# Performance work log

Hardware: AMD Instinct MI355X
Metric: run time of the kernel (lower is better)

The kernel has to match this reference:

```python
import jax, jax.numpy as jnp
import numpy as np

DIM = 3072
NUM_HEADS = 24
HEAD_DIM = 128
SEQ = 2048
BATCH = 1
EPS = 1e-6


def _make_rope(seq_len: int, head_dim: int):
    # Standard RoPE angles; cos/sin laid out per interleaved-pair convention
    # (each frequency repeated for the (real, imag) pair), shape [S, head_dim].
    half = head_dim // 2
    inv_freq = 1.0 / (10000.0 ** (np.arange(0, half, dtype=np.float32) / half))
    t = np.arange(seq_len, dtype=np.float32)
    freqs = np.outer(t, inv_freq)  # [S, half]
    freqs = np.repeat(freqs, 2, axis=-1)  # [S, head_dim], pairs share the angle
    return jnp.asarray(np.cos(freqs)), jnp.asarray(np.sin(freqs))


def setup_inputs() -> dict:
    key = jax.random.key(0)
    ks = jax.random.split(key, 8)
    inner = NUM_HEADS * HEAD_DIM
    s = 0.02
    hidden_states = jax.random.normal(ks[0], (BATCH, SEQ, DIM), dtype=jnp.float32)
    wq = jax.random.normal(ks[1], (inner, DIM), dtype=jnp.float32) * s
    wk = jax.random.normal(ks[2], (inner, DIM), dtype=jnp.float32) * s
    wv = jax.random.normal(ks[3], (inner, DIM), dtype=jnp.float32) * s
    bq = jax.random.normal(ks[4], (inner,), dtype=jnp.float32) * s
    bk = jax.random.normal(ks[5], (inner,), dtype=jnp.float32) * s
    bv = jax.random.normal(ks[6], (inner,), dtype=jnp.float32) * s
    norm_q_w = jnp.ones((HEAD_DIM,), dtype=jnp.float32)
    norm_k_w = jnp.ones((HEAD_DIM,), dtype=jnp.float32)
    cos, sin = _make_rope(SEQ, HEAD_DIM)
    return {
        "hidden_states": hidden_states,
        "wq": wq, "bq": bq, "wk": wk, "bk": bk, "wv": wv, "bv": bv,
        "norm_q_w": norm_q_w, "norm_k_w": norm_k_w,
        "cos": cos, "sin": sin,
    }


def _rms_norm(x, w, eps=EPS):
    # RMSNorm over the last (head_dim) axis.
    var = jnp.mean(jnp.square(x), axis=-1, keepdims=True)
    return x * jax.lax.rsqrt(var + eps) * w


def _apply_rope(x, cos, sin):
    # x: [B, S, H, D]; cos/sin: [S, D]. Interleaved-pair rotation
    # (diffusers apply_rotary_emb, use_real_unbind_dim=-1).
    xr = x[..., 0::2]
    xi = x[..., 1::2]
    rot = jnp.stack([-xi, xr], axis=-1).reshape(x.shape)
    c = cos[None, :, None, :]
    s = sin[None, :, None, :]
    return x * c + rot * s


def reference(hidden_states, wq, bq, wk, bk, wv, bv, norm_q_w, norm_k_w, cos, sin):
    B, S, _ = hidden_states.shape
    H, D = NUM_HEADS, HEAD_DIM
    # QKV projections (ColumnParallelLinear with tp_size=1)
    q = (hidden_states @ wq.T + bq).reshape(B, S, H, D)
    k = (hidden_states @ wk.T + bk).reshape(B, S, H, D)
    v = (hidden_states @ wv.T + bv).reshape(B, S, H, D)
    # qk-norm then RoPE
    q = _apply_rope(_rms_norm(q, norm_q_w), cos, sin)
    k = _apply_rope(_rms_norm(k, norm_k_w), cos, sin)
    # Non-causal full attention
    scale = 1.0 / jnp.sqrt(jnp.asarray(D, dtype=q.dtype))
    scores = jnp.einsum("bqhd,bkhd->bhqk", q, k) * scale
    probs = jax.nn.softmax(scores, axis=-1)
    out = jnp.einsum("bhqk,bkhd->bqhd", probs, v)
    return out.reshape(B, S, H * D).astype(q.dtype)
```

## Files before the change

kernel.cpp:

```cpp
#include <hip/hip_runtime.h>

#define S_LEN 2048
#define DIMSZ 3072
#define NHEAD 24
#define HDIM 128
#define NQKV 9216
#define QSCALE 0.08838834764831845f
#define FMAX 12.0f

typedef unsigned short u16;
typedef unsigned int u32;
typedef __attribute__((ext_vector_type(8))) short short8;
typedef __attribute__((ext_vector_type(4))) float f32x4;

__device__ __forceinline__ u16 f2bf(float f) {
    u32 u = __float_as_uint(f);
    u32 r = (u + 0x7fffu + ((u >> 16) & 1u)) >> 16;
    return (u16)r;
}
__device__ __forceinline__ float bf2f(u16 u) {
    return __uint_as_float((u32)u << 16);
}

__device__ __forceinline__ void lds16(u16* lds, const u16* g) {
    __builtin_amdgcn_global_load_lds((const __attribute__((address_space(1))) u32*)g,
                                     (__attribute__((address_space(3))) u32*)lds, 16, 0, 0);
}

__global__ void k_conv(const float4* __restrict__ hs, const float4* __restrict__ wq,
                       const float4* __restrict__ wk, const float4* __restrict__ wv,
                       u16* __restrict__ hs_b, u16* __restrict__ w_b) {
    int i = blockIdx.x * 256 + threadIdx.x;
    const float4* src;
    u16* dst;
    if (i < 1572864) { src = hs + i; dst = hs_b + (size_t)i * 4; }
    else if (i < 3932160) { src = wq + (i - 1572864); dst = w_b + (size_t)(i - 1572864) * 4; }
    else if (i < 6291456) { src = wk + (i - 3932160); dst = w_b + 9437184 + (size_t)(i - 3932160) * 4; }
    else { src = wv + (i - 6291456); dst = w_b + 18874368 + (size_t)(i - 6291456) * 4; }
    float4 v = *src;
    u32 lo = (u32)f2bf(v.x) | ((u32)f2bf(v.y) << 16);
    u32 hi = (u32)f2bf(v.z) | ((u32)f2bf(v.w) << 16);
    uint2 p; p.x = lo; p.y = hi;
    *(uint2*)dst = p;
}

__global__ __launch_bounds__(256, 2) void k_gemm(const u16* __restrict__ A, const u16* __restrict__ W,
                                                 u16* __restrict__ C) {
    __shared__ __align__(16) u16 As[2][256 * 32];
    __shared__ __align__(16) u16 Bs[2][192 * 32];
    const int tid = threadIdx.x, wave = tid >> 6, lane = tid & 63;
    const int bm = blockIdx.x & 7, bn = blockIdx.x >> 3;
    const int frow = lane & 15, fk = lane >> 4;
    const u16* baseA = A + (size_t)(bm * 256) * DIMSZ;

    auto stageA = [&](int b, int kt) {
#pragma unroll
        for (int j = 0; j < 4; ++j) {
            int flat = j * 256 + tid, row = flat >> 2, ch = flat & 3;
            lds16(&As[b][flat * 8], baseA + (size_t)row * DIMSZ + kt * 32 + ((ch ^ ((row >> 1) & 3)) * 8));
        }
    };
    auto stageB = [&](int b, int kt) {
#pragma unroll
        for (int j = 0; j < 3; ++j) {
            int flat = j * 256 + tid, row = flat >> 2, ch = flat & 3;
            int srow = bn * 144 + row;
            srow = (srow > NQKV - 1) ? (NQKV - 1) : srow;
            lds16(&Bs[b][flat * 8], W + (size_t)srow * DIMSZ + kt * 32 + ((ch ^ ((row >> 1) & 3)) * 8));
        }
    };

    stageA(0, 0); stageB(0, 0); stageA(1, 1); stageB(1, 1);
    asm volatile("s_waitcnt vmcnt(7)");
    __builtin_amdgcn_s_barrier();

    f32x4 acc[4][9] = {};
    for (int T = 0; T < 96; ++T) {
        const int b = T & 1;
        const u16* LA = As[b];
        const u16* LB = Bs[b];
        short8 af[4], bf[9];
#pragma unroll
        for (int mf = 0; mf < 4; ++mf) {
            int row = wave * 64 + mf * 16 + frow;
            af[mf] = *(const short8*)&LA[row * 32 + ((fk ^ ((row >> 1) & 3)) * 8)];
        }
#pragma unroll
        for (int nf = 0; nf < 9; ++nf) {
            int row = nf * 16 + frow;
            bf[nf] = *(const short8*)&LB[row * 32 + ((fk ^ ((row >> 1) & 3)) * 8)];
        }
        __builtin_amdgcn_s_barrier();
        __builtin_amdgcn_s_setprio(1);
#pragma unroll
        for (int mf = 0; mf < 4; ++mf)
#pragma unroll
            for (int nf = 0; nf < 9; ++nf)
                acc[mf][nf] = __builtin_amdgcn_mfma_f32_16x16x32_bf16(af[mf], bf[nf], acc[mf][nf], 0, 0, 0);
        __builtin_amdgcn_s_setprio(0);
        __builtin_amdgcn_s_barrier();
        if (T < 94) {
            stageA(b, T + 2); stageB(b, T + 2);
            asm volatile("s_waitcnt vmcnt(7)");
            __builtin_amdgcn_s_barrier();
        } else if (T == 94) {
            asm volatile("s_waitcnt vmcnt(0)");
            __builtin_amdgcn_s_barrier();
        }
    }

#pragma unroll
    for (int mf = 0; mf < 4; ++mf) {
#pragma unroll
        for (int nf = 0; nf < 9; ++nf) {
            int n = bn * 144 + nf * 16 + frow;
#pragma unroll
            for (int i = 0; i < 4; ++i) {
                int m = bm * 256 + wave * 64 + mf * 16 + fk * 4 + i;
                C[(size_t)m * NQKV + n] = f2bf(acc[mf][nf][i]);
            }
        }
    }
}

__global__ void k_post(const u16* __restrict__ qkv, const float* __restrict__ nw_q,
                       const float* __restrict__ nw_k, const float* __restrict__ bq,
                       const float* __restrict__ bk, const float* __restrict__ bv,
                       const float* __restrict__ cosT, const float* __restrict__ sinT,
                       u16* __restrict__ Qb, u16* __restrict__ Kb, u16* __restrict__ Vt) {
    const int tid = threadIdx.x;
    const int row = blockIdx.x * 16 + (tid >> 4);
    const int lane16 = tid & 15;
    const int s = row & 2047, h = row >> 11;
    const int d0 = lane16 * 8;
    const u16* base = qkv + (size_t)s * NQKV + h * HDIM + d0;

    float cs[8], sn[8];
    *(float4*)&cs[0] = *(const float4*)&cosT[s * HDIM + d0];
    *(float4*)&cs[4] = *(const float4*)&cosT[s * HDIM + d0 + 4];
    *(float4*)&sn[0] = *(const float4*)&sinT[s * HDIM + d0];
    *(float4*)&sn[4] = *(const float4*)&sinT[s * HDIM + d0 + 4];

    {
        short8 raw = *(const short8*)base;
        float b[8];
        *(float4*)&b[0] = *(const float4*)&bq[h * HDIM + d0];
        *(float4*)&b[4] = *(const float4*)&bq[h * HDIM + d0 + 4];
        float x[8], ss = 0.f;
#pragma unroll
        for (int j = 0; j < 8; ++j) { x[j] = bf2f((u16)raw[j]) + b[j]; ss += x[j] * x[j]; }
#pragma unroll
        for (int m = 1; m < 16; m <<= 1) ss += __shfl_xor(ss, m);
        float r = rsqrtf(ss * (1.0f / 128.0f) + 1e-6f);
        float w[8];
        *(float4*)&w[0] = *(const float4*)&nw_q[d0];
        *(float4*)&w[4] = *(const float4*)&nw_q[d0 + 4];
        u32 pk[4];
#pragma unroll
        for (int jp = 0; jp < 4; ++jp) {
            float e = x[2 * jp] * r * w[2 * jp];
            float o = x[2 * jp + 1] * r * w[2 * jp + 1];
            float y0 = (e * cs[2 * jp] - o * sn[2 * jp]) * QSCALE;
            float y1 = (o * cs[2 * jp] + e * sn[2 * jp]) * QSCALE;
            pk[jp] = (u32)f2bf(y0) | ((u32)f2bf(y1) << 16);
        }
        uint4 v; v.x = pk[0]; v.y = pk[1]; v.z = pk[2]; v.w = pk[3];
        *(uint4*)&Qb[((size_t)h * S_LEN + s) * HDIM + d0] = v;
    }
    {
        short8 raw = *(const short8*)(base + 3072);
        float b[8];
        *(float4*)&b[0] = *(const float4*)&bk[h * HDIM + d0];
        *(float4*)&b[4] = *(const float4*)&bk[h * HDIM + d0 + 4];
        float x[8], ss = 0.f;
#pragma unroll
        for (int j = 0; j < 8; ++j) { x[j] = bf2f((u16)raw[j]) + b[j]; ss += x[j] * x[j]; }
#pragma unroll
        for (int m = 1; m < 16; m <<= 1) ss += __shfl_xor(ss, m);
        float r = rsqrtf(ss * (1.0f / 128.0f) + 1e-6f);
        float w[8];
        *(float4*)&w[0] = *(const float4*)&nw_k[d0];
        *(float4*)&w[4] = *(const float4*)&nw_k[d0 + 4];
        u32 pk[4];
#pragma unroll
        for (int jp = 0; jp < 4; ++jp) {
            float e = x[2 * jp] * r * w[2 * jp];
            float o = x[2 * jp + 1] * r * w[2 * jp + 1];
            float y0 = e * cs[2 * jp] - o * sn[2 * jp];
            float y1 = o * cs[2 * jp] + e * sn[2 * jp];
            pk[jp] = (u32)f2bf(y0) | ((u32)f2bf(y1) << 16);
        }
        uint4 v; v.x = pk[0]; v.y = pk[1]; v.z = pk[2]; v.w = pk[3];
        *(uint4*)&Kb[((size_t)h * S_LEN + s) * HDIM + d0] = v;
    }
    {
        short8 raw = *(const short8*)(base + 6144);
        float b[8];
        *(float4*)&b[0] = *(const float4*)&bv[h * HDIM + d0];
        *(float4*)&b[4] = *(const float4*)&bv[h * HDIM + d0 + 4];
#pragma unroll
        for (int j = 0; j < 8; ++j)
            Vt[((size_t)h * HDIM + d0 + j) * S_LEN + s] = f2bf(bf2f((u16)raw[j]) + b[j]);
    }
}

__global__ __launch_bounds__(128, 2) void k_attn(const u16* __restrict__ Qb, const u16* __restrict__ Kb,
                                                 const u16* __restrict__ Vt, float* __restrict__ out) {
    __shared__ __align__(16) u16 Ks[2][32 * 128];
    __shared__ __align__(16) u16 Vs[2][128 * 32];
    __shared__ __align__(16) u16 Ps[2][32 * 32];
    const int tid = threadIdx.x;
    const int wave = tid >> 6, lane = tid & 63;
    const int wg = (blockIdx.x & 7) * 96 + (blockIdx.x >> 3);
    const int h = wg >> 5, qb = wg & 31;
    const int frow = lane & 15, fk = lane >> 4;

    short8 qf[2][4];
#pragma unroll
    for (int qg = 0; qg < 2; ++qg) {
        const u16* qbase = Qb + ((size_t)h * S_LEN + qb * 64 + wave * 32 + qg * 16 + frow) * HDIM + fk * 8;
#pragma unroll
        for (int ks = 0; ks < 4; ++ks) qf[qg][ks] = *(const short8*)(qbase + ks * 32);
    }

    f32x4 o[2][8] = {};
    float l_p[2] = {0.f, 0.f};

#define STAGE(buf, kt)                                                                        \
    {                                                                                         \
        _Pragma("unroll") for (int c = 0; c < 4; ++c) {                                       \
            int flat = c * 128 + tid;                                                         \
            int r = flat >> 4, ch = flat & 15;                                                \
            lds16(Ks[buf] + flat * 8,                                                         \
                  Kb + ((size_t)h * S_LEN + (kt) * 32 + r) * HDIM + ((ch ^ (r & 15)) * 8));   \
        }                                                                                     \
        _Pragma("unroll") for (int c = 0; c < 4; ++c) {                                       \
            int flat = c * 128 + tid;                                                         \
            int r = flat >> 2, ch = flat & 3;                                                 \
            lds16(Vs[buf] + flat * 8,                                                         \
                  Vt + ((size_t)h * HDIM + r) * S_LEN + (kt) * 32 + ((ch ^ ((r >> 2) & 3)) * 8)); \
        }                                                                                     \
    }

    STAGE(0, 0);
    __syncthreads();
    int cur = 0;

    for (int kt = 0; kt < 64; ++kt) {
        if (kt + 1 < 64) STAGE(cur ^ 1, kt + 1);
        f32x4 sacc[2][2] = {};
#pragma unroll
        for (int nf = 0; nf < 2; ++nf) {
#pragma unroll
            for (int ks = 0; ks < 4; ++ks) {
                short8 kf = *(const short8*)&Ks[cur][(nf * 16 + frow) * 128 + (((ks * 4 + fk) ^ frow) * 8)];
#pragma unroll
                for (int qg = 0; qg < 2; ++qg)
                    sacc[qg][nf] = __builtin_amdgcn_mfma_f32_16x16x32_bf16(kf, qf[qg][ks], sacc[qg][nf], 0, 0, 0);
            }
        }
#pragma unroll
        for (int qg = 0; qg < 2; ++qg) {
            int prow = qg * 16 + frow;
#pragma unroll
            for (int nf = 0; nf < 2; ++nf) {
                float p0 = __expf(sacc[qg][nf][0] - FMAX);
                float p1 = __expf(sacc[qg][nf][1] - FMAX);
                float p2 = __expf(sacc[qg][nf][2] - FMAX);
                float p3 = __expf(sacc[qg][nf][3] - FMAX);
                l_p[qg] += (p0 + p1) + (p2 + p3);
                uint2 pk;
                pk.x = (u32)f2bf(p0) | ((u32)f2bf(p1) << 16);
                pk.y = (u32)f2bf(p2) | ((u32)f2bf(p3) << 16);
                int c16 = (nf * 2 + (fk >> 1)) ^ ((prow >> 2) & 3);
                *(uint2*)&Ps[wave][prow * 32 + c16 * 8 + (fk & 1) * 4] = pk;
            }
        }
        short8 pf[2];
#pragma unroll
        for (int qg = 0; qg < 2; ++qg)
            pf[qg] = *(const short8*)&Ps[wave][(qg * 16 + frow) * 32 + ((fk ^ ((frow >> 2) & 3)) * 8)];
#pragma unroll
        for (int nf8 = 0; nf8 < 8; ++nf8) {
            short8 vf = *(const short8*)&Vs[cur][(nf8 * 16 + frow) * 32 + ((fk ^ ((frow >> 2) & 3)) * 8)];
#pragma unroll
            for (int qg = 0; qg < 2; ++qg)
                o[qg][nf8] = __builtin_amdgcn_mfma_f32_16x16x32_bf16(pf[qg], vf, o[qg][nf8], 0, 0, 0);
        }
        __syncthreads();
        cur ^= 1;
    }
#undef STAGE

#pragma unroll
    for (int qg = 0; qg < 2; ++qg) {
        l_p[qg] += __shfl_xor(l_p[qg], 16);
        l_p[qg] += __shfl_xor(l_p[qg], 32);
    }

#pragma unroll
    for (int qg = 0; qg < 2; ++qg)
#pragma unroll
        for (int i = 0; i < 4; ++i) {
            float rinv = 1.0f / __shfl(l_p[qg], fk * 4 + i);
            int srow = qb * 64 + wave * 32 + qg * 16 + fk * 4 + i;
#pragma unroll
            for (int nf8 = 0; nf8 < 8; ++nf8)
                out[(size_t)srow * DIMSZ + h * HDIM + nf8 * 16 + frow] = o[qg][nf8][i] * rinv;
        }
}

extern "C" void kernel_launch(void* const* d_in, const int* in_sizes, int n_in,
                              void* d_out, int out_size, void* d_ws, size_t ws_size,
                              hipStream_t stream) {
    const float* hs = (const float*)d_in[0];
    const float* wq = (const float*)d_in[1];
    const float* bq = (const float*)d_in[2];
    const float* wk = (const float*)d_in[3];
    const float* bk = (const float*)d_in[4];
    const float* wv = (const float*)d_in[5];
    const float* bv = (const float*)d_in[6];
    const float* nq = (const float*)d_in[7];
    const float* nk = (const float*)d_in[8];
    const float* cosT = (const float*)d_in[9];
    const float* sinT = (const float*)d_in[10];
    float* out = (float*)d_out;

    char* ws = (char*)d_ws;
    u16* hs_b = (u16*)(ws);
    u16* w_b = (u16*)(ws + 12582912);
    u16* qkv = (u16*)(ws + 69206016);
    u16* Qb = (u16*)(ws + 106954752);
    u16* Kb = (u16*)(ws + 119537664);
    u16* Vt = (u16*)(ws + 132120576);

    k_conv<<<dim3(33792), 256, 0, stream>>>((const float4*)hs, (const float4*)wq,
                                            (const float4*)wk, (const float4*)wv, hs_b, w_b);

    k_gemm<<<dim3(512), 256, 0, stream>>>(hs_b, w_b, qkv);

    k_post<<<dim3(3072), 256, 0, stream>>>(qkv, nq, nk, bq, bk, bv, cosT, sinT, Qb, Kb, Vt);

    k_attn<<<dim3(768), 128, 0, stream>>>(Qb, Kb, Vt, out);
}
```

Before: 292.1 us.

## Load GEMM B fragments directly from global into registers, bypassing LDS

The B (weight) operand of the QKV GEMM is no longer staged through shared memory. Each wave now reads its MFMA B fragments straight from global memory into registers, one k-step ahead. The loop synchronisation is rebuilt around a full vmcnt(0) wait at the top of each iteration, and the A-tile prefetch is issued before the MFMA block. This cuts LDS traffic and LDS usage per block, but all four waves now read the same B data from global memory, and the full wait shrinks how much load latency is hidden behind compute.

```diff
diff --git a/kernel.cpp b/kernel.cpp
--- a/kernel.cpp
+++ b/kernel.cpp
@@ -47,11 +47,11 @@
 __global__ __launch_bounds__(256, 2) void k_gemm(const u16* __restrict__ A, const u16* __restrict__ W,
                                                  u16* __restrict__ C) {
     __shared__ __align__(16) u16 As[2][256 * 32];
-    __shared__ __align__(16) u16 Bs[2][192 * 32];
     const int tid = threadIdx.x, wave = tid >> 6, lane = tid & 63;
     const int bm = blockIdx.x & 7, bn = blockIdx.x >> 3;
     const int frow = lane & 15, fk = lane >> 4;
     const u16* baseA = A + (size_t)(bm * 256) * DIMSZ;
+    const u16* baseW = W + (size_t)(bn * 144) * DIMSZ;
 
     auto stageA = [&](int b, int kt) {
 #pragma unroll
@@ -60,37 +60,38 @@
             lds16(&As[b][flat * 8], baseA + (size_t)row * DIMSZ + kt * 32 + ((ch ^ ((row >> 1) & 3)) * 8));
         }
     };
-    auto stageB = [&](int b, int kt) {
-#pragma unroll
-        for (int j = 0; j < 3; ++j) {
-            int flat = j * 256 + tid, row = flat >> 2, ch = flat & 3;
-            int srow = bn * 144 + row;
-            srow = (srow > NQKV - 1) ? (NQKV - 1) : srow;
-            lds16(&Bs[b][flat * 8], W + (size_t)srow * DIMSZ + kt * 32 + ((ch ^ ((row >> 1) & 3)) * 8));
-        }
+
+    short8 bf[9];
+    auto loadB = [&](int kt) {
+#pragma unroll
+        for (int nf = 0; nf < 9; ++nf)
+            bf[nf] = *(const short8*)&baseW[(size_t)(nf * 16 + frow) * DIMSZ + kt * 32 + fk * 8];
     };
 
-    stageA(0, 0); stageB(0, 0); stageA(1, 1); stageB(1, 1);
-    asm volatile("s_waitcnt vmcnt(7)");
-    __builtin_amdgcn_s_barrier();
+    stageA(0, 0); stageA(1, 1);
+    loadB(0);
 
     f32x4 acc[4][9] = {};
     for (int T = 0; T < 96; ++T) {
         const int b = T & 1;
+        asm volatile("s_waitcnt vmcnt(0)");
+        __builtin_amdgcn_s_barrier();
+        __builtin_amdgcn_sched_barrier(0);
+
         const u16* LA = As[b];
-        const u16* LB = Bs[b];
-        short8 af[4], bf[9];
+        short8 af[4];
 #pragma unroll
         for (int mf = 0; mf < 4; ++mf) {
             int row = wave * 64 + mf * 16 + frow;
             af[mf] = *(const short8*)&LA[row * 32 + ((fk ^ ((row >> 1) & 3)) * 8)];
         }
-#pragma unroll
-        for (int nf = 0; nf < 9; ++nf) {
-            int row = nf * 16 + frow;
-            bf[nf] = *(const short8*)&LB[row * 32 + ((fk ^ ((row >> 1) & 3)) * 8)];
-        }
+        asm volatile("s_waitcnt lgkmcnt(0)");
+        __builtin_amdgcn_sched_barrier(0);
         __builtin_amdgcn_s_barrier();
+        __builtin_amdgcn_sched_barrier(0);
+
+        if (T < 94) stageA(b, T + 2);
+
         __builtin_amdgcn_s_setprio(1);
 #pragma unroll
         for (int mf = 0; mf < 4; ++mf)
@@ -98,15 +99,8 @@
             for (int nf = 0; nf < 9; ++nf)
                 acc[mf][nf] = __builtin_amdgcn_mfma_f32_16x16x32_bf16(af[mf], bf[nf], acc[mf][nf], 0, 0, 0);
         __builtin_amdgcn_s_setprio(0);
-        __builtin_amdgcn_s_barrier();
-        if (T < 94) {
-            stageA(b, T + 2); stageB(b, T + 2);
-            asm volatile("s_waitcnt vmcnt(7)");
-            __builtin_amdgcn_s_barrier();
-        } else if (T == 94) {
-            asm volatile("s_waitcnt vmcnt(0)");
-            __builtin_amdgcn_s_barrier();
-        }
+
+        if (T < 95) loadB(T + 1);
     }
 
 #pragma unroll
```

Measured after the change: 413.7 us (median of 2 runs). +41.6%, slower.
